# Performance work log

Measured on AMD Instinct MI355X. Metric: run time of the kernel, lower is better.

## Reference

```python
import jax, jax.numpy as jnp
import numpy as np

C = 512
HEADS = 8
HEAD_DIM = C // HEADS
GROUPS = 32
EPS = 1e-5


def group_norm(x, scale, bias):
    b, c, h, w = x.shape
    xg = x.reshape(b, GROUPS, -1)
    mean = xg.mean(axis=-1, keepdims=True)
    var = xg.var(axis=-1, keepdims=True)
    xg = (xg - mean) * jax.lax.rsqrt(var + EPS)
    x = xg.reshape(b, c, h, w)
    return x * scale[None, :, None, None] + bias[None, :, None, None]


def conv1x1(x, w, b):
    # w: (out_c, in_c), x: (B, C, H, W)
    return jnp.einsum('oc,bchw->bohw', w, x) + b[None, :, None, None]


def setup_inputs() -> dict:
    key = jax.random.key(0)
    ks = jax.random.split(key, 11)
    s = 1.0 / np.sqrt(C)
    return {
        'x': jax.random.normal(ks[0], (8, C, 32, 32), jnp.float32),
        'gn_scale': jnp.ones((C,), jnp.float32),
        'gn_bias': jnp.zeros((C,), jnp.float32),
        'wq': jax.random.normal(ks[1], (C, C), jnp.float32) * s,
        'bq': jax.random.normal(ks[2], (C,), jnp.float32) * 0.01,
        'wk': jax.random.normal(ks[3], (C, C), jnp.float32) * s,
        'bk': jax.random.normal(ks[4], (C,), jnp.float32) * 0.01,
        'wv': jax.random.normal(ks[5], (C, C), jnp.float32) * s,
        'bv': jax.random.normal(ks[6], (C,), jnp.float32) * 0.01,
        'wp': jax.random.normal(ks[7], (C, C), jnp.float32) * s,
        'bp': jax.random.normal(ks[8], (C,), jnp.float32) * 0.01,
    }


def reference(x, gn_scale, gn_bias, wq, bq, wk, bk, wv, bv, wp, bp):
    b, c, h, w = x.shape
    n = h * w
    h_in = x
    xn = group_norm(x, gn_scale, gn_bias)
    q = conv1x1(xn, wq, bq).reshape(b, HEADS, HEAD_DIM, n)
    k = conv1x1(xn, wk, bk).reshape(b, HEADS, HEAD_DIM, n)
    v = conv1x1(xn, wv, bv).reshape(b, HEADS, HEAD_DIM, n)
    scale = 1.0 / np.sqrt(HEAD_DIM).astype(np.float32)
    attn = jnp.einsum('bhcn,bhcm->bhnm', q, k) * scale
    attn = jax.nn.softmax(attn, axis=-1)
    out = jnp.einsum('bhnm,bhcm->bhcn', attn, v)
    out = out.reshape(b, c, h, w)
    out = conv1x1(out, wp, bp)
    return out + h_in
```

## Files before the change

kernel.cpp:

```cpp
#include <hip/hip_runtime.h>

#define CC 512
#define NN 1024
#define NB 8
#define NH 8
#define HD 64

typedef __attribute__((ext_vector_type(8))) short s16x8;
typedef __attribute__((ext_vector_type(4))) short s16x4;
typedef __attribute__((ext_vector_type(4))) float f32x4;
typedef __attribute__((ext_vector_type(16))) float f32x16;

__device__ __forceinline__ short f2bf(float f){
  union { float f; unsigned u; } v; v.f = f;
  unsigned r = v.u + 0x7fffu + ((v.u >> 16) & 1u);
  return (short)(r >> 16);
}

__device__ __forceinline__ unsigned cvtpk(float lo, float hi){
  unsigned r;
  asm("v_cvt_pk_bf16_f32 %0, %1, %2" : "=v"(r) : "v"(lo), "v"(hi));
  return r;
}

__device__ __forceinline__ void gload16(const void* g, void* l){
  __builtin_amdgcn_global_load_lds((const __attribute__((address_space(1))) void*)g,
                                   (__attribute__((address_space(3))) void*)l, 16, 0, 0);
}

__global__ __launch_bounds__(256) void wcvt(const float* __restrict__ w0, const float* __restrict__ w1,
    const float* __restrict__ w2, const float* __restrict__ w3, short* __restrict__ wbf){
  const int i = blockIdx.x*256 + threadIdx.x;
  const int sel = i >> 16;
  const int off = (i & 65535) << 2;
  const float* src = (sel==0) ? w0 : (sel==1) ? w1 : (sel==2) ? w2 : w3;
  const float4 v = *reinterpret_cast<const float4*>(src + off);
  s16x4 o;
  o[0] = f2bf(v.x); o[1] = f2bf(v.y); o[2] = f2bf(v.z); o[3] = f2bf(v.w);
  *reinterpret_cast<s16x4*>(wbf + (size_t)sel*262144 + off) = o;
}

__global__ __launch_bounds__(256) void gn_kernel(const float* __restrict__ x,
    const float* __restrict__ gsc, const float* __restrict__ gbi, short* __restrict__ xnt){
  const int b = blockIdx.x >> 5;
  const int g = blockIdx.x & 31;
  const int t = threadIdx.x;
  const float* base = x + ((size_t)b*CC + g*16)*NN;
  float4 vals[16];
  float s = 0.f, s2 = 0.f;
  #pragma unroll
  for (int k = 0; k < 16; ++k){
    float4 v = *reinterpret_cast<const float4*>(base + k*NN + t*4);
    vals[k] = v;
    s  += v.x + v.y + v.z + v.w;
    s2 += v.x*v.x + v.y*v.y + v.z*v.z + v.w*v.w;
  }
  #pragma unroll
  for (int m = 1; m < 64; m <<= 1){ s += __shfl_xor(s, m); s2 += __shfl_xor(s2, m); }
  __shared__ float rs[4], rs2[4];
  const int wid = t >> 6, lane = t & 63;
  if (lane == 0){ rs[wid] = s; rs2[wid] = s2; }
  __syncthreads();
  s  = rs[0] + rs[1] + rs[2] + rs[3];
  s2 = rs2[0] + rs2[1] + rs2[2] + rs2[3];
  const float mean = s * (1.f/16384.f);
  const float inv = rsqrtf(s2 * (1.f/16384.f) - mean*mean + 1e-5f);
  float scl[16], off[16];
  #pragma unroll
  for (int k = 0; k < 16; ++k){
    const float sc = gsc[g*16 + k] * inv;
    scl[k] = sc;
    off[k] = gbi[g*16 + k] - mean * sc;
  }
  short* obase = xnt + ((size_t)b*NN + t*4)*CC + g*16;
  #pragma unroll
  for (int i = 0; i < 4; ++i){
    s16x8 lo, hi;
    #pragma unroll
    for (int k = 0; k < 8; ++k){
      float v = (i==0) ? vals[k].x : (i==1) ? vals[k].y : (i==2) ? vals[k].z : vals[k].w;
      lo[k] = f2bf(v * scl[k] + off[k]);
    }
    #pragma unroll
    for (int k = 0; k < 8; ++k){
      float v = (i==0) ? vals[k+8].x : (i==1) ? vals[k+8].y : (i==2) ? vals[k+8].z : vals[k+8].w;
      hi[k] = f2bf(v * scl[k+8] + off[k+8]);
    }
    *reinterpret_cast<s16x8*>(obase + (size_t)i*CC)     = lo;
    *reinterpret_cast<s16x8*>(obase + (size_t)i*CC + 8) = hi;
  }
}

template<int MODE>
__global__ __launch_bounds__(256) void gemm_kernel(
    const short* __restrict__ Wb, const short* __restrict__ Bmat,
    const float* __restrict__ bias0, const float* __restrict__ bias1, const float* __restrict__ bias2,
    const float* __restrict__ resid,
    short* __restrict__ qt, short* __restrict__ kt2, short* __restrict__ vo,
    float* __restrict__ outp)
{
  const int tile = blockIdx.x;
  const int batch = blockIdx.y;
  const int z = blockIdx.z;
  const int mt = tile >> 3, nt = tile & 7;
  const int tid = threadIdx.x;
  const int lane = tid & 63, wid = tid >> 6;
  const int wm = wid >> 1, wn = wid & 1;

  __shared__ short As[2][128*64];
  __shared__ short Bs[2][128*64];

  const short* Wz = Wb + (size_t)(MODE == 0 ? z : 3) * 262144;
  const short* Brow = Bmat + ((size_t)batch*NN + nt*128)*CC;

  const f32x4 fzero = {0.f, 0.f, 0.f, 0.f};
  f32x4 acc[4][4];
  #pragma unroll
  for (int i = 0; i < 4; ++i)
  #pragma unroll
  for (int j = 0; j < 4; ++j)
    acc[i][j] = fzero;

  const int srow = tid >> 3, sch = tid & 7;
  const int sgch = sch ^ (srow & 7);

  auto stage = [&](int kk, int buf){
    #pragma unroll
    for (int j = 0; j < 4; ++j){
      const int row = srow + 32*j;
      gload16(Wz   + (size_t)(mt*128 + row)*CC + kk*64 + sgch*8, &As[buf][(wid*64 + 256*j)*8]);
      gload16(Brow + (size_t)row*CC            + kk*64 + sgch*8, &Bs[buf][(wid*64 + 256*j)*8]);
    }
  };

  auto compute = [&](int buf){
    #pragma unroll
    for (int ks = 0; ks < 2; ++ks){
      s16x8 a[4], b[4];
      #pragma unroll
      for (int mi = 0; mi < 4; ++mi){
        const int row = wm*64 + mi*16 + (lane & 15);
        const int ch = (ks*4 + (lane >> 4)) ^ (row & 7);
        a[mi] = *reinterpret_cast<const s16x8*>(&As[buf][row*64 + ch*8]);
      }
      #pragma unroll
      for (int ni = 0; ni < 4; ++ni){
        const int row = wn*64 + ni*16 + (lane & 15);
        const int ch = (ks*4 + (lane >> 4)) ^ (row & 7);
        b[ni] = *reinterpret_cast<const s16x8*>(&Bs[buf][row*64 + ch*8]);
      }
      if (MODE == 0 && z == 2){
        #pragma unroll
        for (int mi = 0; mi < 4; ++mi)
        #pragma unroll
        for (int ni = 0; ni < 4; ++ni)
          acc[mi][ni] = __builtin_amdgcn_mfma_f32_16x16x32_bf16(b[ni], a[mi], acc[mi][ni], 0, 0, 0);
      } else {
        #pragma unroll
        for (int mi = 0; mi < 4; ++mi)
        #pragma unroll
        for (int ni = 0; ni < 4; ++ni)
          acc[mi][ni] = __builtin_amdgcn_mfma_f32_16x16x32_bf16(a[mi], b[ni], acc[mi][ni], 0, 0, 0);
      }
    }
  };

  stage(0, 0);
  __syncthreads();
  #pragma unroll
  for (int kk = 0; kk < 8; kk += 2){
    if (kk + 1 < 8) stage(kk + 1, 1);
    compute(0);
    __syncthreads();
    if (kk + 2 < 8) stage(kk + 2, 0);
    compute(1);
    __syncthreads();
  }

  const int obase = mt*128 + wm*64;
  const int nbase = nt*128 + wn*64;
  if (MODE == 0){
    const int head = mt*2 + wm;
    const size_t hb = ((size_t)batch*NH + head)*65536;
    const int hi2 = (lane >> 5) & 1;
    const int j0 = ((lane >> 4) & 1)*4;
    if (z < 2){
      const float* bias = (z == 0) ? bias0 : bias1;
      short* dst = (z == 0) ? qt : kt2;
      const float qs = (z == 0) ? 0.125f * 1.44269504f : 1.0f;
      #pragma unroll
      for (int mi = 0; mi < 4; ++mi){
        float bv4[4];
        #pragma unroll
        for (int r = 0; r < 4; ++r) bv4[r] = bias[obase + mi*16 + (lane>>4)*4 + r];
        #pragma unroll
        for (int ni = 0; ni < 4; ++ni){
          const int l = (ni & 1)*16 + (lane & 15) + 32*hi2;
          const int q5 = nt*4 + wn*2 + (ni >> 1);
          s16x4 pk;
          #pragma unroll
          for (int r = 0; r < 4; ++r) pk[r] = f2bf((acc[mi][ni][r] + bv4[r]) * qs);
          *reinterpret_cast<s16x4*>(dst + hb + (size_t)((q5*4 + mi)*64 + l)*8 + j0) = pk;
        }
      }
    } else {
      #pragma unroll
      for (int mi = 0; mi < 4; ++mi){
        const float bv = bias2[obase + mi*16 + (lane & 15)];
        const int ci = mi >> 1;
        const int cl = (mi & 1)*16 + (lane & 15);
        #pragma unroll
        for (int ni = 0; ni < 4; ++ni){
          const int m5 = nt*2 + wn;
          s16x4 pk;
          #pragma unroll
          for (int r = 0; r < 4; ++r) pk[r] = f2bf(acc[mi][ni][r] + bv);
          *reinterpret_cast<s16x4*>(vo + hb + (size_t)((((ci*16 + m5)*4 + ni)*64) + cl + 32*hi2)*8 + j0) = pk;
        }
      }
    }
  } else {
    #pragma unroll
    for (int mi = 0; mi < 4; ++mi){
      float bv4[4];
      #pragma unroll
      for (int r = 0; r < 4; ++r) bv4[r] = bias0[obase + mi*16 + (lane>>4)*4 + r];
      #pragma unroll
      for (int ni = 0; ni < 4; ++ni){
        const int n = nbase + ni*16 + (lane & 15);
        #pragma unroll
        for (int r = 0; r < 4; ++r){
          const int o = obase + mi*16 + (lane>>4)*4 + r;
          const size_t idx = ((size_t)batch*CC + o)*NN + n;
          outp[idx] = acc[mi][ni][r] + bv4[r] + resid[idx];
        }
      }
    }
  }
}

__global__ __launch_bounds__(256, 2) void attn_kernel(
    const short* __restrict__ qp, const short* __restrict__ kp, const short* __restrict__ vp,
    short* __restrict__ ot)
{
  const int bid = blockIdx.x;
  const int xcd = bid & 7, rr = bid >> 3;
  const int bh  = xcd*8 + (rr & 7);
  const int qt  = rr >> 3;
  const int b = bh >> 3, head = bh & 7;
  const int tid = threadIdx.x, lane = tid & 63, wid = tid >> 6;
  const int col = lane & 31;
  const int qg = wid & 1, kh = wid >> 1;
  const int q0 = qt*64 + qg*32;

  const short* Qf = qp + (size_t)bh*65536;
  const short* Kf = kp + (size_t)bh*65536;
  const short* Vf = vp + (size_t)bh*65536;

  __shared__ float Lof[2][32][64];
  __shared__ float Lm[2][64];
  __shared__ float Ll[2][64];

  const int q5 = qt*2 + qg;
  s16x8 qf[4];
  #pragma unroll
  for (int ks = 0; ks < 4; ++ks)
    qf[ks] = *reinterpret_cast<const s16x8*>(Qf + (size_t)(q5*4 + ks)*512 + lane*8);

  f32x16 of0, of1;
  #pragma unroll
  for (int r = 0; r < 16; ++r){ of0[r] = 0.f; of1[r] = 0.f; }
  float m = -1e30f, l = 0.f;

  auto kload = [&](int itn, s16x8 (&kf)[2][4]){
    const short* kb = Kf + (size_t)(kh*16 + itn*2)*2048 + lane*8;
    #pragma unroll
    for (int t = 0; t < 2; ++t)
      #pragma unroll
      for (int ks = 0; ks < 4; ++ks)
        kf[t][ks] = *reinterpret_cast<const s16x8*>(kb + t*2048 + ks*512);
  };

  auto pack = [&](f32x16& sv, s16x8& p0, s16x8& p1){
    union { unsigned u[4]; s16x8 v; } w0, w1;
    {
      unsigned a = cvtpk(sv[0], sv[1]);
      unsigned c = cvtpk(sv[4], sv[5]);
      auto r = __builtin_amdgcn_permlane32_swap(a, c, false, false);
      w0.u[0] = r[0]; w0.u[2] = r[1];
      a = cvtpk(sv[2], sv[3]);
      c = cvtpk(sv[6], sv[7]);
      r = __builtin_amdgcn_permlane32_swap(a, c, false, false);
      w0.u[1] = r[0]; w0.u[3] = r[1];
    }
    {
      unsigned a = cvtpk(sv[8], sv[9]);
      unsigned c = cvtpk(sv[12], sv[13]);
      auto r = __builtin_amdgcn_permlane32_swap(a, c, false, false);
      w1.u[0] = r[0]; w1.u[2] = r[1];
      a = cvtpk(sv[10], sv[11]);
      c = cvtpk(sv[14], sv[15]);
      r = __builtin_amdgcn_permlane32_swap(a, c, false, false);
      w1.u[1] = r[0]; w1.u[3] = r[1];
    }
    p0 = w0.v; p1 = w1.v;
  };

  auto body = [&](int it, s16x8 (&kf)[2][4], s16x8 (&kfn)[2][4]){
    const int m5 = kh*8 + it;
    s16x8 vf[2][4];
    const short* vb = Vf + (size_t)m5*2048 + lane*8;
    #pragma unroll
    for (int ci = 0; ci < 2; ++ci)
      #pragma unroll
      for (int s = 0; s < 4; ++s)
        vf[ci][s] = *reinterpret_cast<const s16x8*>(vb + ci*32768 + s*512);
    f32x16 s0, s1;
    #pragma unroll
    for (int r = 0; r < 16; ++r){ s0[r] = 0.f; s1[r] = 0.f; }
    __builtin_amdgcn_s_setprio(1);
    #pragma unroll
    for (int ks = 0; ks < 4; ++ks){
      s0 = __builtin_amdgcn_mfma_f32_32x32x16_bf16(kf[0][ks], qf[ks], s0, 0, 0, 0);
      s1 = __builtin_amdgcn_mfma_f32_32x32x16_bf16(kf[1][ks], qf[ks], s1, 0, 0, 0);
    }
    __builtin_amdgcn_s_setprio(0);
    if (it < 7) kload(it + 1, kfn);
    float t[16];
    #pragma unroll
    for (int r = 0; r < 16; ++r) t[r] = fmaxf(s0[r], s1[r]);
    #pragma unroll
    for (int o = 8; o > 0; o >>= 1)
      #pragma unroll
      for (int r = 0; r < 8; ++r) if (r < o) t[r] = fmaxf(t[r], t[r + o]);
    float tm = fmaxf(t[0], __shfl_xor(t[0], 32));
    const float mn = fmaxf(m, tm);
    const float sc = __builtin_amdgcn_exp2f(m - mn);
    m = mn;
    #pragma unroll
    for (int r = 0; r < 16; ++r){ s0[r] = __builtin_amdgcn_exp2f(s0[r] - mn); }
    #pragma unroll
    for (int r = 0; r < 16; ++r){ s1[r] = __builtin_amdgcn_exp2f(s1[r] - mn); }
    #pragma unroll
    for (int r = 0; r < 16; ++r) t[r] = s0[r] + s1[r];
    #pragma unroll
    for (int o = 8; o > 0; o >>= 1)
      #pragma unroll
      for (int r = 0; r < 8; ++r) if (r < o) t[r] = t[r] + t[r + o];
    float rs = t[0] + __shfl_xor(t[0], 32);
    l = l*sc + rs;
    #pragma unroll
    for (int r = 0; r < 16; ++r){ of0[r] *= sc; of1[r] *= sc; }
    s16x8 pf[4];
    pack(s0, pf[0], pf[1]);
    pack(s1, pf[2], pf[3]);
    __builtin_amdgcn_s_setprio(1);
    #pragma unroll
    for (int s = 0; s < 4; ++s){
      of0 = __builtin_amdgcn_mfma_f32_32x32x16_bf16(vf[0][s], pf[s], of0, 0, 0, 0);
      of1 = __builtin_amdgcn_mfma_f32_32x32x16_bf16(vf[1][s], pf[s], of1, 0, 0, 0);
    }
    __builtin_amdgcn_s_setprio(0);
  };

  s16x8 kfA[2][4], kfB[2][4];
  kload(0, kfA);
  #pragma unroll 1
  for (int ii = 0; ii < 4; ++ii){
    body(2*ii,     kfA, kfB);
    body(2*ii + 1, kfB, kfA);
  }

  __syncthreads();
  if (kh == 1){
    #pragma unroll
    for (int r = 0; r < 16; ++r){
      Lof[qg][r][lane]      = of0[r];
      Lof[qg][16 + r][lane] = of1[r];
    }
    Lm[qg][lane] = m;
    Ll[qg][lane] = l;
  }
  __syncthreads();
  if (kh == 0){
    const float m1 = Lm[qg][lane], l1 = Ll[qg][lane];
    const float mn = fmaxf(m, m1);
    const float a0 = __builtin_amdgcn_exp2f(m - mn);
    const float a1 = __builtin_amdgcn_exp2f(m1 - mn);
    const float linv = 1.f / (l*a0 + l1*a1);
    const int hi = lane >> 5;
    const int n = q0 + col;
    short* ob = ot + ((size_t)b*NN + n)*CC + head*HD + hi*4;
    #pragma unroll
    for (int rq = 0; rq < 4; ++rq){
      s16x4 pk;
      #pragma unroll
      for (int r = 0; r < 4; ++r)
        pk[r] = f2bf((of0[rq*4 + r]*a0 + Lof[qg][rq*4 + r][lane]*a1) * linv);
      *reinterpret_cast<s16x4*>(ob + rq*8) = pk;
      #pragma unroll
      for (int r = 0; r < 4; ++r)
        pk[r] = f2bf((of1[rq*4 + r]*a0 + Lof[qg][16 + rq*4 + r][lane]*a1) * linv);
      *reinterpret_cast<s16x4*>(ob + 32 + rq*8) = pk;
    }
  }
}

extern "C" void kernel_launch(void* const* d_in, const int* in_sizes, int n_in,
                              void* d_out, int out_size, void* d_ws, size_t ws_size,
                              hipStream_t stream) {
  const float* x   = (const float*)d_in[0];
  const float* gsc = (const float*)d_in[1];
  const float* gbi = (const float*)d_in[2];
  const float* wq  = (const float*)d_in[3];
  const float* bq  = (const float*)d_in[4];
  const float* wk  = (const float*)d_in[5];
  const float* bk  = (const float*)d_in[6];
  const float* wv  = (const float*)d_in[7];
  const float* bv  = (const float*)d_in[8];
  const float* wp  = (const float*)d_in[9];
  const float* bp  = (const float*)d_in[10];
  float* out = (float*)d_out;

  char* ws = (char*)d_ws;
  short* wbf = (short*)(ws);
  short* xnt = (short*)(ws + (2u<<20));
  short* qt  = (short*)(ws + (10u<<20));
  short* kt  = (short*)(ws + (18u<<20));
  short* v   = (short*)(ws + (26u<<20));
  short* aot = (short*)(ws + (34u<<20));

  wcvt<<<1024, 256, 0, stream>>>(wq, wk, wv, wp, wbf);
  gn_kernel<<<256, 256, 0, stream>>>(x, gsc, gbi, xnt);
  gemm_kernel<0><<<dim3(32, 8, 3), 256, 0, stream>>>(wbf, xnt, bq, bk, bv, nullptr,
                                                     qt, kt, v, nullptr);
  attn_kernel<<<dim3(1024), 256, 0, stream>>>(qt, kt, v, aot);
  gemm_kernel<1><<<dim3(32, 8, 1), 256, 0, stream>>>(wbf, aot, bp, nullptr, nullptr, x,
                                                     nullptr, nullptr, nullptr, out);
}
```

Measured before the change: 88.50 us.

## Merge weight-convert and groupnorm kernels; halve GEMM k-tile with vmcnt-based pipelining

Fuses the weight bf16 conversion and group-norm kernels into one launch, using the block index to choose the role, which removes one kernel launch. The GEMM k-tile shrinks from 64 to 32 so LDS use per block is halved, and the XOR swizzle is adjusted to the narrower rows. The loop now runs 16 steps and waits with s_waitcnt vmcnt(4) plus raw barriers so the next tile's loads stay in flight while the current tile is computed. The cost is twice as many barriers per k step and less MFMA work between each synchronisation.

```diff
diff --git a/kernel.cpp b/kernel.cpp
--- a/kernel.cpp
+++ b/kernel.cpp
@@ -28,22 +28,25 @@
                                    (__attribute__((address_space(3))) void*)l, 16, 0, 0);
 }
 
-__global__ __launch_bounds__(256) void wcvt(const float* __restrict__ w0, const float* __restrict__ w1,
-    const float* __restrict__ w2, const float* __restrict__ w3, short* __restrict__ wbf){
-  const int i = blockIdx.x*256 + threadIdx.x;
-  const int sel = i >> 16;
-  const int off = (i & 65535) << 2;
-  const float* src = (sel==0) ? w0 : (sel==1) ? w1 : (sel==2) ? w2 : w3;
-  const float4 v = *reinterpret_cast<const float4*>(src + off);
-  s16x4 o;
-  o[0] = f2bf(v.x); o[1] = f2bf(v.y); o[2] = f2bf(v.z); o[3] = f2bf(v.w);
-  *reinterpret_cast<s16x4*>(wbf + (size_t)sel*262144 + off) = o;
-}
-
-__global__ __launch_bounds__(256) void gn_kernel(const float* __restrict__ x,
-    const float* __restrict__ gsc, const float* __restrict__ gbi, short* __restrict__ xnt){
-  const int b = blockIdx.x >> 5;
-  const int g = blockIdx.x & 31;
+__global__ __launch_bounds__(256) void prep_kernel(const float* __restrict__ x,
+    const float* __restrict__ gsc, const float* __restrict__ gbi,
+    const float* __restrict__ w0, const float* __restrict__ w1,
+    const float* __restrict__ w2, const float* __restrict__ w3,
+    short* __restrict__ wbf, short* __restrict__ xnt){
+  if (blockIdx.x < 1024){
+    const int i = blockIdx.x*256 + threadIdx.x;
+    const int sel = i >> 16;
+    const int off = (i & 65535) << 2;
+    const float* src = (sel==0) ? w0 : (sel==1) ? w1 : (sel==2) ? w2 : w3;
+    const float4 v = *reinterpret_cast<const float4*>(src + off);
+    s16x4 o;
+    o[0] = f2bf(v.x); o[1] = f2bf(v.y); o[2] = f2bf(v.z); o[3] = f2bf(v.w);
+    *reinterpret_cast<s16x4*>(wbf + (size_t)sel*262144 + off) = o;
+    return;
+  }
+  const int blk = blockIdx.x - 1024;
+  const int b = blk >> 5;
+  const int g = blk & 31;
   const int t = threadIdx.x;
   const float* base = x + ((size_t)b*CC + g*16)*NN;
   float4 vals[16];
@@ -107,8 +110,8 @@
   const int lane = tid & 63, wid = tid >> 6;
   const int wm = wid >> 1, wn = wid & 1;
 
-  __shared__ short As[2][128*64];
-  __shared__ short Bs[2][128*64];
+  __shared__ short As[2][128*32];
+  __shared__ short Bs[2][128*32];
 
   const short* Wz = Wb + (size_t)(MODE == 0 ? z : 3) * 262144;
   const short* Brow = Bmat + ((size_t)batch*NN + nt*128)*CC;
@@ -121,60 +124,63 @@
   for (int j = 0; j < 4; ++j)
     acc[i][j] = fzero;
 
-  const int srow = tid >> 3, sch = tid & 7;
-  const int sgch = sch ^ (srow & 7);
+  const int srow = tid >> 2, sh = tid & 3;
+  const int sg = sh ^ ((srow >> 1) & 3);
+  const short* gaBase = Wz + (size_t)(mt*128 + srow)*CC + sg*8;
+  const short* gbBase = Brow + (size_t)srow*CC + sg*8;
 
   auto stage = [&](int kk, int buf){
-    #pragma unroll
-    for (int j = 0; j < 4; ++j){
-      const int row = srow + 32*j;
-      gload16(Wz   + (size_t)(mt*128 + row)*CC + kk*64 + sgch*8, &As[buf][(wid*64 + 256*j)*8]);
-      gload16(Brow + (size_t)row*CC            + kk*64 + sgch*8, &Bs[buf][(wid*64 + 256*j)*8]);
-    }
+    const short* ga = gaBase + kk*32;
+    const short* gb = gbBase + kk*32;
+    gload16(ga,          &As[buf][tid*8]);
+    gload16(ga + 64*CC,  &As[buf][(tid + 256)*8]);
+    gload16(gb,          &Bs[buf][tid*8]);
+    gload16(gb + 64*CC,  &Bs[buf][(tid + 256)*8]);
   };
 
+  const int rch = ((lane >> 4) ^ (((lane & 15) >> 1) & 3));
+
   auto compute = [&](int buf){
-    #pragma unroll
-    for (int ks = 0; ks < 2; ++ks){
-      s16x8 a[4], b[4];
-      #pragma unroll
-      for (int mi = 0; mi < 4; ++mi){
-        const int row = wm*64 + mi*16 + (lane & 15);
-        const int ch = (ks*4 + (lane >> 4)) ^ (row & 7);
-        a[mi] = *reinterpret_cast<const s16x8*>(&As[buf][row*64 + ch*8]);
-      }
-      #pragma unroll
-      for (int ni = 0; ni < 4; ++ni){
-        const int row = wn*64 + ni*16 + (lane & 15);
-        const int ch = (ks*4 + (lane >> 4)) ^ (row & 7);
-        b[ni] = *reinterpret_cast<const s16x8*>(&Bs[buf][row*64 + ch*8]);
-      }
-      if (MODE == 0 && z == 2){
-        #pragma unroll
-        for (int mi = 0; mi < 4; ++mi)
-        #pragma unroll
-        for (int ni = 0; ni < 4; ++ni)
-          acc[mi][ni] = __builtin_amdgcn_mfma_f32_16x16x32_bf16(b[ni], a[mi], acc[mi][ni], 0, 0, 0);
-      } else {
-        #pragma unroll
-        for (int mi = 0; mi < 4; ++mi)
-        #pragma unroll
-        for (int ni = 0; ni < 4; ++ni)
-          acc[mi][ni] = __builtin_amdgcn_mfma_f32_16x16x32_bf16(a[mi], b[ni], acc[mi][ni], 0, 0, 0);
-      }
+    s16x8 a[4], b[4];
+    #pragma unroll
+    for (int mi = 0; mi < 4; ++mi){
+      const int row = wm*64 + mi*16 + (lane & 15);
+      a[mi] = *reinterpret_cast<const s16x8*>(&As[buf][row*32 + rch*8]);
+    }
+    #pragma unroll
+    for (int ni = 0; ni < 4; ++ni){
+      const int row = wn*64 + ni*16 + (lane & 15);
+      b[ni] = *reinterpret_cast<const s16x8*>(&Bs[buf][row*32 + rch*8]);
+    }
+    if (MODE == 0 && z == 2){
+      #pragma unroll
+      for (int mi = 0; mi < 4; ++mi)
+      #pragma unroll
+      for (int ni = 0; ni < 4; ++ni)
+        acc[mi][ni] = __builtin_amdgcn_mfma_f32_16x16x32_bf16(b[ni], a[mi], acc[mi][ni], 0, 0, 0);
+    } else {
+      #pragma unroll
+      for (int mi = 0; mi < 4; ++mi)
+      #pragma unroll
+      for (int ni = 0; ni < 4; ++ni)
+        acc[mi][ni] = __builtin_amdgcn_mfma_f32_16x16x32_bf16(a[mi], b[ni], acc[mi][ni], 0, 0, 0);
     }
   };
 
   stage(0, 0);
-  __syncthreads();
-  #pragma unroll
-  for (int kk = 0; kk < 8; kk += 2){
-    if (kk + 1 < 8) stage(kk + 1, 1);
-    compute(0);
-    __syncthreads();
-    if (kk + 2 < 8) stage(kk + 2, 0);
-    compute(1);
-    __syncthreads();
+  #pragma unroll
+  for (int kk = 0; kk < 16; ++kk){
+    const int buf = kk & 1;
+    if (kk < 15){
+      stage(kk + 1, buf ^ 1);
+      asm volatile("s_waitcnt vmcnt(4)" ::: "memory");
+    } else {
+      asm volatile("s_waitcnt vmcnt(0)" ::: "memory");
+    }
+    __builtin_amdgcn_s_barrier();
+    compute(buf);
+    asm volatile("" ::: "memory");
+    __builtin_amdgcn_s_barrier();
   }
 
   const int obase = mt*128 + wm*64;
@@ -430,8 +436,7 @@
   short* v   = (short*)(ws + (26u<<20));
   short* aot = (short*)(ws + (34u<<20));
 
-  wcvt<<<1024, 256, 0, stream>>>(wq, wk, wv, wp, wbf);
-  gn_kernel<<<256, 256, 0, stream>>>(x, gsc, gbi, xnt);
+  prep_kernel<<<1280, 256, 0, stream>>>(x, gsc, gbi, wq, wk, wv, wp, wbf, xnt);
   gemm_kernel<0><<<dim3(32, 8, 3), 256, 0, stream>>>(wbf, xnt, bq, bk, bv, nullptr,
                                                      qt, kt, v, nullptr);
   attn_kernel<<<dim3(1024), 256, 0, stream>>>(qt, kt, v, aot);
```

Measured after the change: 96.78 us. 9.4% more time.
